# Kernel tuning notes

Hardware: AMD Instinct MI355X
Metric: run time of the kernel (lower is better)

Reference implementation:

```python
import jax, jax.numpy as jnp
import numpy as np

T, B, D, H = 4096, 4, 1024, 8
EPS = 1e-5


def _ln(z, g, b):
    m = jnp.mean(z, axis=-1, keepdims=True)
    v = jnp.mean((z - m) ** 2, axis=-1, keepdims=True)
    return (z - m) * jax.lax.rsqrt(v + EPS) * g + b


def setup_inputs() -> dict:
    key = jax.random.key(0)
    ks = jax.random.split(key, 8)
    s = 0.02
    return {
        "x": jax.random.normal(ks[0], (T, B, D), dtype=jnp.float32),
        "norm_w": jnp.ones((D,), jnp.float32),
        "norm_b": jnp.zeros((D,), jnp.float32),
        "tnorm_w": jnp.ones((D,), jnp.float32),
        "tnorm_b": jnp.zeros((D,), jnp.float32),
        "Wq": jax.random.normal(ks[1], (D, D), jnp.float32) * s,
        "bq": jnp.zeros((D,), jnp.float32),
        "Wk": jax.random.normal(ks[2], (D, D), jnp.float32) * s,
        "bk": jnp.zeros((D,), jnp.float32),
        "Wv": jax.random.normal(ks[3], (D, D), jnp.float32) * s,
        "bv": jnp.zeros((D,), jnp.float32),
    }


def reference(x, norm_w, norm_b, tnorm_w, tnorm_b, Wq, bq, Wk, bk, Wv, bv):
    # x: (T, B, D) -> (B, T, D), matching torch x.permute(1, 0, 2)
    xb = jnp.transpose(x, (1, 0, 2))
    b, t, d = xb.shape
    hd = d // H
    xn = _ln(xb, norm_w, norm_b)          # query branch norm
    xtn = _ln(xb, tnorm_w, tnorm_b)       # key/value branch norm (text_norm applied to x)
    q = (xn @ Wq.T + bq).reshape(b, t, H, hd)
    k = (xtn @ Wk.T + bk).reshape(b, t, H, hd)
    v = (xtn @ Wv.T + bv).reshape(b, t, H, hd)
    q = jax.nn.softmax(q, axis=-1)        # softmax over head-dim
    k = jax.nn.softmax(k, axis=1)         # softmax over time
    # kv state: (B, H, hd, hd)
    att = jnp.einsum('bthd,bthl->bhdl', k, v)
    y = jnp.einsum('bthd,bhdl->bthl', q, att).reshape(b, t, d)
    return y  # original forward returns y directly (proj_out/dropout unused)
```

## Files before the change

kernel.cpp:

```cpp
#include <hip/hip_runtime.h>
#include <cstdint>

#define T_LEN 4096
#define BATCH 4
#define DIM   1024
#define NH    8
#define HDIM  128
#define ROWS  16384

typedef __bf16 bf16x8 __attribute__((ext_vector_type(8)));
typedef float  f32x4  __attribute__((ext_vector_type(4)));

__device__ __forceinline__ unsigned short f2bf(float f) {
  union { float f; unsigned u; } a; a.f = f;
  unsigned u = a.u;
  u += 0x7fff + ((u >> 16) & 1);
  return (unsigned short)(u >> 16);
}
__device__ __forceinline__ float bf2f(unsigned short h) {
  union { unsigned u; float f; } a; a.u = ((unsigned)h) << 16;
  return a.f;
}

__device__ __forceinline__ void gld_lds16(const unsigned short* g, unsigned short* l) {
  __builtin_amdgcn_global_load_lds(
      (const __attribute__((address_space(1))) unsigned int*)g,
      (__attribute__((address_space(3))) unsigned int*)l, 16, 0, 0);
}

__global__ __launch_bounds__(256) void ln_kernel(
    const float* __restrict__ x, const float* __restrict__ nw, const float* __restrict__ nb,
    const float* __restrict__ tw, const float* __restrict__ tb,
    unsigned short* __restrict__ xn, unsigned short* __restrict__ xtn) {
  int row = blockIdx.x;
  int t = row >> 2, b = row & 3;
  int tid = threadIdx.x;
  const float4 v = ((const float4*)(x + (size_t)row * DIM))[tid];
  float s  = v.x + v.y + v.z + v.w;
  float s2 = v.x*v.x + v.y*v.y + v.z*v.z + v.w*v.w;
#pragma unroll
  for (int o = 32; o; o >>= 1) { s += __shfl_xor(s, o); s2 += __shfl_xor(s2, o); }
  __shared__ float red[8];
  int wv = tid >> 6;
  if ((tid & 63) == 0) { red[wv] = s; red[4 + wv] = s2; }
  __syncthreads();
  s  = red[0] + red[1] + red[2] + red[3];
  s2 = red[4] + red[5] + red[6] + red[7];
  float mean = s * (1.0f / DIM);
  float var  = s2 * (1.0f / DIM) - mean * mean;
  float rstd = rsqrtf(var + 1e-5f);
  size_t orow = ((size_t)b * T_LEN + t) * DIM;
  int c0 = tid * 4;
  float xv[4] = {v.x, v.y, v.z, v.w};
  union { unsigned short u[4]; uint2 d; } o1, o2;
#pragma unroll
  for (int j = 0; j < 4; ++j) {
    int c = c0 + j;
    float xh = (xv[j] - mean) * rstd;
    o1.u[j] = f2bf(xh * nw[c] + nb[c]);
    o2.u[j] = f2bf(xh * tw[c] + tb[c]);
  }
  *(uint2*)(xn  + orow + c0) = o1.d;
  *(uint2*)(xtn + orow + c0) = o2.d;
}

__global__ __launch_bounds__(256) void wconv(
    const float* __restrict__ Wq, const float* __restrict__ Wk, const float* __restrict__ Wv,
    unsigned short* __restrict__ out) {
  int i4 = blockIdx.x * 256 + threadIdx.x;
  int w = i4 >> 18;
  const float* src = (w == 0) ? Wq : (w == 1 ? Wk : Wv);
  float4 v = ((const float4*)src)[i4 & 262143];
  union { unsigned short u[4]; uint2 d; } o;
  o.u[0] = f2bf(v.x); o.u[1] = f2bf(v.y); o.u[2] = f2bf(v.z); o.u[3] = f2bf(v.w);
  ((uint2*)out)[i4] = o.d;
}

__global__ __launch_bounds__(256) void qkv_gemm(
    const unsigned short* __restrict__ xn, const unsigned short* __restrict__ xtn,
    const unsigned short* __restrict__ wbf,
    const float* __restrict__ bq, const float* __restrict__ bk, const float* __restrict__ bv,
    unsigned short* __restrict__ qo, unsigned short* __restrict__ ko, unsigned short* __restrict__ vo) {
  int z = blockIdx.z;
  const unsigned short* A = (z == 0) ? xn : xtn;
  const unsigned short* W = wbf + (size_t)z * DIM * DIM;
  const float* bias = (z == 0) ? bq : (z == 1 ? bk : bv);
  unsigned short* outp = (z == 0) ? qo : (z == 1 ? ko : vo);

  int m0t = blockIdx.x * 128;
  int n0 = blockIdx.y * 128;
  __shared__ __align__(16) unsigned short As[128 * 64];
  __shared__ __align__(16) unsigned short Bs[128 * 64];
  int tid = threadIdx.x;
  int wave = tid >> 6, lane = tid & 63;
  int wm = (wave >> 1) * 64, wn = (wave & 1) * 64;
  int l16 = lane & 15, kq = lane >> 4;
  int swz = l16 & 7;

  int srow = tid >> 3;
  int skk  = (((tid & 7) ^ ((tid >> 3) & 7)) * 8);
  const unsigned short* Ag = A + (size_t)(m0t + srow) * DIM + skk;
  const unsigned short* Wg = W + (size_t)(n0 + srow) * DIM + skk;
  unsigned short* Al = As + wave * 512;
  unsigned short* Bl = Bs + wave * 512;

  f32x4 acc[4][4] = {};

  for (int kt = 0; kt < DIM; kt += 64) {
#pragma unroll
    for (int p = 0; p < 4; ++p) {
      gld_lds16(Ag + (size_t)(p * 32) * DIM + kt, Al + p * 2048);
      gld_lds16(Wg + (size_t)(p * 32) * DIM + kt, Bl + p * 2048);
    }
    __syncthreads();
#pragma unroll
    for (int ks4 = 0; ks4 < 2; ++ks4) {
      int coff = (((kq + ks4 * 4) ^ swz) * 8);
      bf16x8 fa[4], fb[4];
#pragma unroll
      for (int i = 0; i < 4; ++i) {
        fa[i] = *(const bf16x8*)(As + (wm + i * 16 + l16) * 64 + coff);
        fb[i] = *(const bf16x8*)(Bs + (wn + i * 16 + l16) * 64 + coff);
      }
#pragma unroll
      for (int i = 0; i < 4; ++i)
#pragma unroll
        for (int j = 0; j < 4; ++j)
          acc[i][j] = __builtin_amdgcn_mfma_f32_16x16x32_bf16(fa[i], fb[j], acc[i][j], 0, 0, 0);
    }
    __syncthreads();
  }

  float bcol[4];
#pragma unroll
  for (int j = 0; j < 4; ++j) bcol[j] = bias[n0 + wn + j * 16 + l16];
#pragma unroll
  for (int i = 0; i < 4; ++i)
#pragma unroll
    for (int j = 0; j < 4; ++j)
#pragma unroll
      for (int r = 0; r < 4; ++r) acc[i][j][r] += bcol[j];

  if (z == 0) {
    float* redm = (float*)As;
    float* reds = redm + 256;
#pragma unroll
    for (int i = 0; i < 4; ++i) {
#pragma unroll
      for (int r = 0; r < 4; ++r) {
        float pm = acc[i][0][r];
#pragma unroll
        for (int j = 1; j < 4; ++j) pm = fmaxf(pm, acc[i][j][r]);
        pm = fmaxf(pm, __shfl_xor(pm, 1));
        pm = fmaxf(pm, __shfl_xor(pm, 2));
        pm = fmaxf(pm, __shfl_xor(pm, 4));
        pm = fmaxf(pm, __shfl_xor(pm, 8));
        float ps = 0.0f;
#pragma unroll
        for (int j = 0; j < 4; ++j) ps += __expf(acc[i][j][r] - pm);
        ps += __shfl_xor(ps, 1);
        ps += __shfl_xor(ps, 2);
        ps += __shfl_xor(ps, 4);
        ps += __shfl_xor(ps, 8);
        if (l16 == 0) {
          int lrow = wm + i * 16 + kq * 4 + r;
          redm[lrow * 2 + (wave & 1)] = pm;
          reds[lrow * 2 + (wave & 1)] = ps;
        }
      }
    }
    __syncthreads();
#pragma unroll
    for (int i = 0; i < 4; ++i) {
#pragma unroll
      for (int r = 0; r < 4; ++r) {
        int lrow = wm + i * 16 + kq * 4 + r;
        float ma = redm[lrow * 2], mb = redm[lrow * 2 + 1];
        float sa = reds[lrow * 2], sb = reds[lrow * 2 + 1];
        float M = fmaxf(ma, mb);
        float inv = 1.0f / (sa * __expf(ma - M) + sb * __expf(mb - M));
        size_t gr = (size_t)(m0t + lrow) * DIM;
#pragma unroll
        for (int j = 0; j < 4; ++j) {
          int col = n0 + wn + j * 16 + l16;
          outp[gr + col] = f2bf(__expf(acc[i][j][r] - M) * inv);
        }
      }
    }
  } else {
    int b = m0t >> 12;
    int tb = m0t & 4095;
    unsigned short* obase = outp + (size_t)b * DIM * T_LEN + tb;
    bool doExp = (z == 1);
#pragma unroll
    for (int j = 0; j < 4; ++j) {
      int col = n0 + wn + j * 16 + l16;
      unsigned short* cp = obase + (size_t)col * T_LEN;
#pragma unroll
      for (int i = 0; i < 4; ++i) {
        int t0 = wm + i * 16 + kq * 4;
#pragma unroll
        for (int r = 0; r < 4; ++r) {
          float val = acc[i][j][r];
          cp[t0 + r] = f2bf(doExp ? __expf(val) : val);
        }
      }
    }
  }
}

__global__ __launch_bounds__(256) void zsum(
    const unsigned short* __restrict__ ksmT, float* __restrict__ Zk) {
  int row = blockIdx.x;
  const unsigned short* p = ksmT + (size_t)row * T_LEN + threadIdx.x * 16;
  uint4 a = *(const uint4*)p;
  uint4 bq = *(const uint4*)(p + 8);
  const unsigned short* ua = (const unsigned short*)&a;
  const unsigned short* ub = (const unsigned short*)&bq;
  float s = 0.0f;
#pragma unroll
  for (int j = 0; j < 8; ++j) s += bf2f(ua[j]) + bf2f(ub[j]);
#pragma unroll
  for (int o = 32; o; o >>= 1) s += __shfl_xor(s, o);
  __shared__ float red[4];
  int wv = threadIdx.x >> 6;
  if ((threadIdx.x & 63) == 0) red[wv] = s;
  __syncthreads();
  if (threadIdx.x == 0) Zk[row] = red[0] + red[1] + red[2] + red[3];
}

__global__ __launch_bounds__(256) void att_gemm(
    const unsigned short* __restrict__ vT, const unsigned short* __restrict__ ksmT,
    float* __restrict__ attT) {
  int kc = blockIdx.x;
  int bh = blockIdx.y;
  const unsigned short* Arow = vT   + (size_t)bh * HDIM * T_LEN;
  const unsigned short* Brow = ksmT + (size_t)bh * HDIM * T_LEN;
  __shared__ __align__(16) unsigned short As[128 * 64];
  __shared__ __align__(16) unsigned short Bs[128 * 64];
  int tid = threadIdx.x;
  int wave = tid >> 6, lane = tid & 63;
  int wm = (wave >> 1) * 64, wn = (wave & 1) * 64;
  int l16 = lane & 15, kq = lane >> 4;
  int swz = l16 & 7;
  int srow = tid >> 3;
  int skk = (((tid & 7) ^ ((tid >> 3) & 7)) * 8);
  const unsigned short* Ag = Arow + (size_t)srow * T_LEN + skk;
  const unsigned short* Bg = Brow + (size_t)srow * T_LEN + skk;
  unsigned short* Al = As + wave * 512;
  unsigned short* Bl = Bs + wave * 512;
  f32x4 acc[4][4] = {};
  int kbeg = kc * 512;
  for (int kt = kbeg; kt < kbeg + 512; kt += 64) {
#pragma unroll
    for (int p = 0; p < 4; ++p) {
      gld_lds16(Ag + (size_t)(p * 32) * T_LEN + kt, Al + p * 2048);
      gld_lds16(Bg + (size_t)(p * 32) * T_LEN + kt, Bl + p * 2048);
    }
    __syncthreads();
#pragma unroll
    for (int ks4 = 0; ks4 < 2; ++ks4) {
      int coff = (((kq + ks4 * 4) ^ swz) * 8);
      bf16x8 fa[4], fb[4];
#pragma unroll
      for (int i = 0; i < 4; ++i) {
        fa[i] = *(const bf16x8*)(As + (wm + i * 16 + l16) * 64 + coff);
        fb[i] = *(const bf16x8*)(Bs + (wn + i * 16 + l16) * 64 + coff);
      }
#pragma unroll
      for (int i = 0; i < 4; ++i)
#pragma unroll
        for (int j = 0; j < 4; ++j)
          acc[i][j] = __builtin_amdgcn_mfma_f32_16x16x32_bf16(fa[i], fb[j], acc[i][j], 0, 0, 0);
    }
    __syncthreads();
  }
#pragma unroll
  for (int j = 0; j < 4; ++j) {
    int col = wn + j * 16 + l16;
#pragma unroll
    for (int i = 0; i < 4; ++i) {
      int rb = wm + i * 16 + kq * 4;
#pragma unroll
      for (int r = 0; r < 4; ++r)
        atomicAdd(attT + (size_t)bh * 16384 + (size_t)(rb + r) * 128 + col, acc[i][j][r]);
    }
  }
}

__global__ __launch_bounds__(256) void attcvt(
    const float* __restrict__ attT, const float* __restrict__ Zk,
    unsigned short* __restrict__ attbf) {
  int idx = blockIdx.x * 256 + threadIdx.x;
  int bh = idx >> 14;
  int b = bh >> 3, h = bh & 7;
  int d = idx & 127;
  float z = Zk[b * DIM + h * HDIM + d];
  attbf[idx] = f2bf(attT[idx] / z);
}

__global__ __launch_bounds__(256) void y_gemm(
    const unsigned short* __restrict__ qsm, const unsigned short* __restrict__ attbf,
    float* __restrict__ out) {
  int h = blockIdx.y;
  int m0t = blockIdx.x * 128;
  int b = m0t >> 12;
  int bh = b * 8 + h;
  const unsigned short* Brow = attbf + (size_t)bh * 16384;
  __shared__ __align__(16) unsigned short As[128 * 64];
  __shared__ __align__(16) unsigned short Bs[128 * 64];
  int tid = threadIdx.x;
  int wave = tid >> 6, lane = tid & 63;
  int wm = (wave >> 1) * 64, wn = (wave & 1) * 64;
  int l16 = lane & 15, kq = lane >> 4;
  int swz = l16 & 7;
  int srow = tid >> 3;
  int skk = (((tid & 7) ^ ((tid >> 3) & 7)) * 8);
  const unsigned short* Ag = qsm + (size_t)(m0t + srow) * DIM + h * HDIM + skk;
  const unsigned short* Bg = Brow + (size_t)srow * HDIM + skk;
  unsigned short* Al = As + wave * 512;
  unsigned short* Bl = Bs + wave * 512;
  f32x4 acc[4][4] = {};
  for (int kt = 0; kt < HDIM; kt += 64) {
#pragma unroll
    for (int p = 0; p < 4; ++p) {
      gld_lds16(Ag + (size_t)(p * 32) * DIM + kt, Al + p * 2048);
      gld_lds16(Bg + (size_t)(p * 32) * HDIM + kt, Bl + p * 2048);
    }
    __syncthreads();
#pragma unroll
    for (int ks4 = 0; ks4 < 2; ++ks4) {
      int coff = (((kq + ks4 * 4) ^ swz) * 8);
      bf16x8 fa[4], fb[4];
#pragma unroll
      for (int i = 0; i < 4; ++i) {
        fa[i] = *(const bf16x8*)(As + (wm + i * 16 + l16) * 64 + coff);
        fb[i] = *(const bf16x8*)(Bs + (wn + i * 16 + l16) * 64 + coff);
      }
#pragma unroll
      for (int i = 0; i < 4; ++i)
#pragma unroll
        for (int j = 0; j < 4; ++j)
          acc[i][j] = __builtin_amdgcn_mfma_f32_16x16x32_bf16(fa[i], fb[j], acc[i][j], 0, 0, 0);
    }
    __syncthreads();
  }
#pragma unroll
  for (int j = 0; j < 4; ++j) {
    int col = wn + j * 16 + l16;
#pragma unroll
    for (int i = 0; i < 4; ++i) {
      int rb = wm + i * 16 + kq * 4;
#pragma unroll
      for (int r = 0; r < 4; ++r)
        out[(size_t)(m0t + rb + r) * DIM + h * HDIM + col] = acc[i][j][r];
    }
  }
}

extern "C" void kernel_launch(void* const* d_in, const int* in_sizes, int n_in,
                              void* d_out, int out_size, void* d_ws, size_t ws_size,
                              hipStream_t stream) {
  const float* x  = (const float*)d_in[0];
  const float* nw = (const float*)d_in[1];
  const float* nb = (const float*)d_in[2];
  const float* tw = (const float*)d_in[3];
  const float* tb = (const float*)d_in[4];
  const float* Wq = (const float*)d_in[5];
  const float* bq = (const float*)d_in[6];
  const float* Wk = (const float*)d_in[7];
  const float* bk = (const float*)d_in[8];
  const float* Wv = (const float*)d_in[9];
  const float* bv = (const float*)d_in[10];
  float* out = (float*)d_out;

  char* ws = (char*)d_ws;
  unsigned short* xn   = (unsigned short*)(ws);
  unsigned short* xtn  = (unsigned short*)(ws + 33554432);
  unsigned short* q    = (unsigned short*)(ws + 67108864);
  unsigned short* ksmT = (unsigned short*)(ws + 100663296);
  unsigned short* vT   = (unsigned short*)(ws + 134217728);
  unsigned short* wbf  = (unsigned short*)(ws + 167772160);
  float* attT          = (float*)(ws + 174063616);
  unsigned short* attbf= (unsigned short*)(ws + 176160768);
  float* Zk            = (float*)(ws + 177209344);

  ln_kernel<<<ROWS, 256, 0, stream>>>(x, nw, nb, tw, tb, xn, xtn);
  wconv<<<3072, 256, 0, stream>>>(Wq, Wk, Wv, wbf);
  qkv_gemm<<<dim3(128, 8, 3), 256, 0, stream>>>(xn, xtn, wbf, bq, bk, bv, q, ksmT, vT);
  zsum<<<4096, 256, 0, stream>>>(ksmT, Zk);
  (void)hipMemsetAsync(attT, 0, 32 * 128 * 128 * 4, stream);
  att_gemm<<<dim3(8, 32), 256, 0, stream>>>(vT, ksmT, attT);
  attcvt<<<2048, 256, 0, stream>>>(attT, Zk, attbf);
  y_gemm<<<dim3(128, 8), 256, 0, stream>>>(q, attbf, out);
}
```

Measured before the change: 339.5 us.

## Enlarge QKV GEMM tile to 256x256 with double-buffered LDS pipeline

Reworks the QKV projection GEMM to use 512-thread blocks computing 256x256 output tiles. Global-to-LDS loads go through a two-stage double buffer with explicit vmcnt waits, and s_setprio is set around the MFMA bursts. The goal is to overlap memory loads with MFMA work and to raise data reuse per byte loaded. The V/K transposed output stores are packed into 8-byte vector writes. The change uses 128KB of LDS and 128 accumulator registers per lane, which limits occupancy to one block per CU and spreads the head-dim softmax reduction across wave pairs.

```diff
diff --git a/kernel.cpp b/kernel.cpp
--- a/kernel.cpp
+++ b/kernel.cpp
@@ -76,7 +76,7 @@
   ((uint2*)out)[i4] = o.d;
 }
 
-__global__ __launch_bounds__(256) void qkv_gemm(
+__global__ __launch_bounds__(512, 2) void qkv_gemm(
     const unsigned short* __restrict__ xn, const unsigned short* __restrict__ xtn,
     const unsigned short* __restrict__ wbf,
     const float* __restrict__ bq, const float* __restrict__ bk, const float* __restrict__ bv,
@@ -87,109 +87,135 @@
   const float* bias = (z == 0) ? bq : (z == 1 ? bk : bv);
   unsigned short* outp = (z == 0) ? qo : (z == 1 ? ko : vo);
 
-  int m0t = blockIdx.x * 128;
-  int n0 = blockIdx.y * 128;
-  __shared__ __align__(16) unsigned short As[128 * 64];
-  __shared__ __align__(16) unsigned short Bs[128 * 64];
+  int m0 = blockIdx.x * 256;
+  int n0 = blockIdx.y * 256;
+
+  __shared__ __align__(16) unsigned short lds[65536];
+
   int tid = threadIdx.x;
   int wave = tid >> 6, lane = tid & 63;
-  int wm = (wave >> 1) * 64, wn = (wave & 1) * 64;
+  int wr = wave >> 2, wc = wave & 3;
+  int wm = wr * 128, wn = wc * 64;
   int l16 = lane & 15, kq = lane >> 4;
   int swz = l16 & 7;
 
   int srow = tid >> 3;
   int skk  = (((tid & 7) ^ ((tid >> 3) & 7)) * 8);
-  const unsigned short* Ag = A + (size_t)(m0t + srow) * DIM + skk;
+  const unsigned short* Ag = A + (size_t)(m0 + srow) * DIM + skk;
   const unsigned short* Wg = W + (size_t)(n0 + srow) * DIM + skk;
-  unsigned short* Al = As + wave * 512;
-  unsigned short* Bl = Bs + wave * 512;
-
-  f32x4 acc[4][4] = {};
-
-  for (int kt = 0; kt < DIM; kt += 64) {
+
+  f32x4 acc[8][4] = {};
+
+  auto stage = [&](int tt, int sb) {
+    int kt = tt * 64;
 #pragma unroll
     for (int p = 0; p < 4; ++p) {
-      gld_lds16(Ag + (size_t)(p * 32) * DIM + kt, Al + p * 2048);
-      gld_lds16(Wg + (size_t)(p * 32) * DIM + kt, Bl + p * 2048);
-    }
-    __syncthreads();
-#pragma unroll
-    for (int ks4 = 0; ks4 < 2; ++ks4) {
+      gld_lds16(Ag + (size_t)(p * 64) * DIM + kt, lds + sb + p * 4096 + wave * 512);
+      gld_lds16(Wg + (size_t)(p * 64) * DIM + kt, lds + 32768 + sb + p * 4096 + wave * 512);
+    }
+  };
+
+  stage(0, 0);
+  stage(1, 16384);
+
+  for (int t = 0; t < 16; ++t) {
+    int sb = (t & 1) ? 16384 : 0;
+    const unsigned short* As = lds + sb;
+    const unsigned short* Bs = lds + 32768 + sb;
+
+    if (t < 15) asm volatile("s_waitcnt vmcnt(8)" ::: "memory");
+    else        asm volatile("s_waitcnt vmcnt(0)" ::: "memory");
+    __builtin_amdgcn_sched_barrier(0);
+    __builtin_amdgcn_s_barrier();
+    __builtin_amdgcn_sched_barrier(0);
+
+#pragma unroll
+    for (int ph = 0; ph < 4; ++ph) {
+      int mh = ph & 1, ks4 = ph >> 1;
       int coff = (((kq + ks4 * 4) ^ swz) * 8);
       bf16x8 fa[4], fb[4];
 #pragma unroll
       for (int i = 0; i < 4; ++i) {
-        fa[i] = *(const bf16x8*)(As + (wm + i * 16 + l16) * 64 + coff);
+        fa[i] = *(const bf16x8*)(As + (wm + (mh * 4 + i) * 16 + l16) * 64 + coff);
         fb[i] = *(const bf16x8*)(Bs + (wn + i * 16 + l16) * 64 + coff);
       }
+      __builtin_amdgcn_s_barrier();
+      __builtin_amdgcn_s_setprio(1);
 #pragma unroll
       for (int i = 0; i < 4; ++i)
 #pragma unroll
         for (int j = 0; j < 4; ++j)
-          acc[i][j] = __builtin_amdgcn_mfma_f32_16x16x32_bf16(fa[i], fb[j], acc[i][j], 0, 0, 0);
-    }
-    __syncthreads();
-  }
-
-  float bcol[4];
-#pragma unroll
-  for (int j = 0; j < 4; ++j) bcol[j] = bias[n0 + wn + j * 16 + l16];
-#pragma unroll
-  for (int i = 0; i < 4; ++i)
-#pragma unroll
-    for (int j = 0; j < 4; ++j)
-#pragma unroll
-      for (int r = 0; r < 4; ++r) acc[i][j][r] += bcol[j];
+          acc[mh * 4 + i][j] =
+              __builtin_amdgcn_mfma_f32_16x16x32_bf16(fa[i], fb[j], acc[mh * 4 + i][j], 0, 0, 0);
+      __builtin_amdgcn_s_setprio(0);
+      __builtin_amdgcn_s_barrier();
+    }
+
+    asm volatile("" ::: "memory");
+    __builtin_amdgcn_sched_barrier(0);
+    if (t < 14) stage(t + 2, sb);
+    __builtin_amdgcn_sched_barrier(0);
+  }
+
+#pragma unroll
+  for (int j = 0; j < 4; ++j) {
+    float bc = bias[n0 + wn + j * 16 + l16];
+#pragma unroll
+    for (int ii = 0; ii < 8; ++ii)
+#pragma unroll
+      for (int r = 0; r < 4; ++r) acc[ii][j][r] += bc;
+  }
 
   if (z == 0) {
-    float* redm = (float*)As;
-    float* reds = redm + 256;
-#pragma unroll
-    for (int i = 0; i < 4; ++i) {
+    float* redm = (float*)lds;
+    float* reds = redm + 1024;
+#pragma unroll
+    for (int ii = 0; ii < 8; ++ii) {
 #pragma unroll
       for (int r = 0; r < 4; ++r) {
-        float pm = acc[i][0][r];
-#pragma unroll
-        for (int j = 1; j < 4; ++j) pm = fmaxf(pm, acc[i][j][r]);
+        float pm = acc[ii][0][r];
+#pragma unroll
+        for (int j = 1; j < 4; ++j) pm = fmaxf(pm, acc[ii][j][r]);
         pm = fmaxf(pm, __shfl_xor(pm, 1));
         pm = fmaxf(pm, __shfl_xor(pm, 2));
         pm = fmaxf(pm, __shfl_xor(pm, 4));
         pm = fmaxf(pm, __shfl_xor(pm, 8));
         float ps = 0.0f;
 #pragma unroll
-        for (int j = 0; j < 4; ++j) ps += __expf(acc[i][j][r] - pm);
+        for (int j = 0; j < 4; ++j) ps += __expf(acc[ii][j][r] - pm);
         ps += __shfl_xor(ps, 1);
         ps += __shfl_xor(ps, 2);
         ps += __shfl_xor(ps, 4);
         ps += __shfl_xor(ps, 8);
         if (l16 == 0) {
-          int lrow = wm + i * 16 + kq * 4 + r;
-          redm[lrow * 2 + (wave & 1)] = pm;
-          reds[lrow * 2 + (wave & 1)] = ps;
+          int row = wm + ii * 16 + kq * 4 + r;
+          redm[row * 4 + wc] = pm;
+          reds[row * 4 + wc] = ps;
         }
       }
     }
     __syncthreads();
 #pragma unroll
-    for (int i = 0; i < 4; ++i) {
+    for (int ii = 0; ii < 8; ++ii) {
 #pragma unroll
       for (int r = 0; r < 4; ++r) {
-        int lrow = wm + i * 16 + kq * 4 + r;
-        float ma = redm[lrow * 2], mb = redm[lrow * 2 + 1];
-        float sa = reds[lrow * 2], sb = reds[lrow * 2 + 1];
+        int row = wm + ii * 16 + kq * 4 + r;
+        int pb = wc & 2;
+        float ma = redm[row * 4 + pb], mb = redm[row * 4 + pb + 1];
+        float sa = reds[row * 4 + pb], sb2 = reds[row * 4 + pb + 1];
         float M = fmaxf(ma, mb);
-        float inv = 1.0f / (sa * __expf(ma - M) + sb * __expf(mb - M));
-        size_t gr = (size_t)(m0t + lrow) * DIM;
+        float inv = 1.0f / (sa * __expf(ma - M) + sb2 * __expf(mb - M));
+        size_t gr = (size_t)(m0 + row) * DIM;
 #pragma unroll
         for (int j = 0; j < 4; ++j) {
           int col = n0 + wn + j * 16 + l16;
-          outp[gr + col] = f2bf(__expf(acc[i][j][r] - M) * inv);
+          outp[gr + col] = f2bf(__expf(acc[ii][j][r] - M) * inv);
         }
       }
     }
   } else {
-    int b = m0t >> 12;
-    int tb = m0t & 4095;
+    int b = m0 >> 12;
+    int tb = m0 & 4095;
     unsigned short* obase = outp + (size_t)b * DIM * T_LEN + tb;
     bool doExp = (z == 1);
 #pragma unroll
@@ -197,13 +223,15 @@
       int col = n0 + wn + j * 16 + l16;
       unsigned short* cp = obase + (size_t)col * T_LEN;
 #pragma unroll
-      for (int i = 0; i < 4; ++i) {
-        int t0 = wm + i * 16 + kq * 4;
+      for (int ii = 0; ii < 8; ++ii) {
+        int t0 = wm + ii * 16 + kq * 4;
+        union { unsigned short u[4]; uint2 d; } o;
 #pragma unroll
         for (int r = 0; r < 4; ++r) {
-          float val = acc[i][j][r];
-          cp[t0 + r] = f2bf(doExp ? __expf(val) : val);
+          float val = acc[ii][j][r];
+          o.u[r] = f2bf(doExp ? __expf(val) : val);
         }
+        *(uint2*)(cp + t0) = o.d;
       }
     }
   }
@@ -387,7 +415,7 @@
 
   ln_kernel<<<ROWS, 256, 0, stream>>>(x, nw, nb, tw, tb, xn, xtn);
   wconv<<<3072, 256, 0, stream>>>(Wq, Wk, Wv, wbf);
-  qkv_gemm<<<dim3(128, 8, 3), 256, 0, stream>>>(xn, xtn, wbf, bq, bk, bv, q, ksmT, vT);
+  qkv_gemm<<<dim3(64, 4, 3), 512, 0, stream>>>(xn, xtn, wbf, bq, bk, bv, q, ksmT, vT);
   zsum<<<4096, 256, 0, stream>>>(ksmT, Zk);
   (void)hipMemsetAsync(attT, 0, 32 * 128 * 128 * 4, stream);
   att_gemm<<<dim3(8, 32), 256, 0, stream>>>(vT, ksmT, attT);
```

After: 333.9 us. About the same (-1.7%).

## Double-buffer QKV GEMM, fuse weight conversion into LN, fold Z sums into epilogue

Applied to the files above, without the earlier changes.

The QKV GEMM now runs 512-thread blocks over 256-row tiles with a K-step of 32. Two LDS buffers are filled asynchronously and explicit vmcnt waits plus barriers overlap loads with MFMA. The weight bf16 conversion becomes extra blocks of the LayerNorm kernel, and the separate zsum pass is replaced by per-column exp sums reduced with shuffles and atomically added into Zk in the GEMM epilogue. The K/V stores are also vectorised into 8-byte writes. This removes two launches and a full reread of the key tensor, at the cost of atomics and the risk that the hand-tuned waitcnt pipeline is fragile.

```diff
diff --git a/kernel.cpp b/kernel.cpp
--- a/kernel.cpp
+++ b/kernel.cpp
@@ -28,13 +28,25 @@
       (__attribute__((address_space(3))) unsigned int*)l, 16, 0, 0);
 }
 
-__global__ __launch_bounds__(256) void ln_kernel(
+__global__ __launch_bounds__(256) void lnw_kernel(
     const float* __restrict__ x, const float* __restrict__ nw, const float* __restrict__ nb,
     const float* __restrict__ tw, const float* __restrict__ tb,
-    unsigned short* __restrict__ xn, unsigned short* __restrict__ xtn) {
+    unsigned short* __restrict__ xn, unsigned short* __restrict__ xtn,
+    const float* __restrict__ Wq, const float* __restrict__ Wk, const float* __restrict__ Wv,
+    unsigned short* __restrict__ wbf) {
+  int tid = threadIdx.x;
+  if (blockIdx.x >= ROWS) {
+    int i4 = (blockIdx.x - ROWS) * 256 + tid;
+    int w = i4 >> 18;
+    const float* src = (w == 0) ? Wq : (w == 1 ? Wk : Wv);
+    float4 v = ((const float4*)src)[i4 & 262143];
+    union { unsigned short u[4]; uint2 d; } o;
+    o.u[0] = f2bf(v.x); o.u[1] = f2bf(v.y); o.u[2] = f2bf(v.z); o.u[3] = f2bf(v.w);
+    ((uint2*)wbf)[i4] = o.d;
+    return;
+  }
   int row = blockIdx.x;
   int t = row >> 2, b = row & 3;
-  int tid = threadIdx.x;
   const float4 v = ((const float4*)(x + (size_t)row * DIM))[tid];
   float s  = v.x + v.y + v.z + v.w;
   float s2 = v.x*v.x + v.y*v.y + v.z*v.z + v.w*v.w;
@@ -64,86 +76,89 @@
   *(uint2*)(xtn + orow + c0) = o2.d;
 }
 
-__global__ __launch_bounds__(256) void wconv(
-    const float* __restrict__ Wq, const float* __restrict__ Wk, const float* __restrict__ Wv,
-    unsigned short* __restrict__ out) {
-  int i4 = blockIdx.x * 256 + threadIdx.x;
-  int w = i4 >> 18;
-  const float* src = (w == 0) ? Wq : (w == 1 ? Wk : Wv);
-  float4 v = ((const float4*)src)[i4 & 262143];
-  union { unsigned short u[4]; uint2 d; } o;
-  o.u[0] = f2bf(v.x); o.u[1] = f2bf(v.y); o.u[2] = f2bf(v.z); o.u[3] = f2bf(v.w);
-  ((uint2*)out)[i4] = o.d;
-}
-
-__global__ __launch_bounds__(256) void qkv_gemm(
+__global__ __launch_bounds__(512, 4) void qkv_gemm(
     const unsigned short* __restrict__ xn, const unsigned short* __restrict__ xtn,
     const unsigned short* __restrict__ wbf,
     const float* __restrict__ bq, const float* __restrict__ bk, const float* __restrict__ bv,
-    unsigned short* __restrict__ qo, unsigned short* __restrict__ ko, unsigned short* __restrict__ vo) {
+    unsigned short* __restrict__ qo, unsigned short* __restrict__ ko, unsigned short* __restrict__ vo,
+    float* __restrict__ Zk) {
   int z = blockIdx.z;
   const unsigned short* A = (z == 0) ? xn : xtn;
   const unsigned short* W = wbf + (size_t)z * DIM * DIM;
   const float* bias = (z == 0) ? bq : (z == 1 ? bk : bv);
   unsigned short* outp = (z == 0) ? qo : (z == 1 ? ko : vo);
 
-  int m0t = blockIdx.x * 128;
+  int m0 = blockIdx.x * 256;
   int n0 = blockIdx.y * 128;
-  __shared__ __align__(16) unsigned short As[128 * 64];
-  __shared__ __align__(16) unsigned short Bs[128 * 64];
+
+  __shared__ __align__(16) unsigned short lds[24576];
+
   int tid = threadIdx.x;
   int wave = tid >> 6, lane = tid & 63;
-  int wm = (wave >> 1) * 64, wn = (wave & 1) * 64;
+  int wr = wave >> 1, wc = wave & 1;
+  int wm = wr * 64, wn = wc * 64;
   int l16 = lane & 15, kq = lane >> 4;
-  int swz = l16 & 7;
-
-  int srow = tid >> 3;
-  int skk  = (((tid & 7) ^ ((tid >> 3) & 7)) * 8);
-  const unsigned short* Ag = A + (size_t)(m0t + srow) * DIM + skk;
-  const unsigned short* Wg = W + (size_t)(n0 + srow) * DIM + skk;
-  unsigned short* Al = As + wave * 512;
-  unsigned short* Bl = Bs + wave * 512;
+  int rs = (kq ^ (l16 & 3)) * 8;
+
+  int arow = tid >> 2;
+  int achk = (tid & 3) ^ (arow & 3);
+  const unsigned short* Ag = A + (size_t)(m0 + arow) * DIM + achk * 8;
+  const unsigned short* Wg = W + (size_t)(n0 + arow) * DIM + achk * 8;
 
   f32x4 acc[4][4] = {};
 
-  for (int kt = 0; kt < DIM; kt += 64) {
-#pragma unroll
-    for (int p = 0; p < 4; ++p) {
-      gld_lds16(Ag + (size_t)(p * 32) * DIM + kt, Al + p * 2048);
-      gld_lds16(Wg + (size_t)(p * 32) * DIM + kt, Bl + p * 2048);
-    }
-    __syncthreads();
-#pragma unroll
-    for (int ks4 = 0; ks4 < 2; ++ks4) {
-      int coff = (((kq + ks4 * 4) ^ swz) * 8);
-      bf16x8 fa[4], fb[4];
-#pragma unroll
-      for (int i = 0; i < 4; ++i) {
-        fa[i] = *(const bf16x8*)(As + (wm + i * 16 + l16) * 64 + coff);
-        fb[i] = *(const bf16x8*)(Bs + (wn + i * 16 + l16) * 64 + coff);
-      }
-#pragma unroll
-      for (int i = 0; i < 4; ++i)
-#pragma unroll
-        for (int j = 0; j < 4; ++j)
-          acc[i][j] = __builtin_amdgcn_mfma_f32_16x16x32_bf16(fa[i], fb[j], acc[i][j], 0, 0, 0);
-    }
-    __syncthreads();
-  }
-
-  float bcol[4];
-#pragma unroll
-  for (int j = 0; j < 4; ++j) bcol[j] = bias[n0 + wn + j * 16 + l16];
-#pragma unroll
-  for (int i = 0; i < 4; ++i)
-#pragma unroll
-    for (int j = 0; j < 4; ++j)
-#pragma unroll
-      for (int r = 0; r < 4; ++r) acc[i][j][r] += bcol[j];
+  auto stage = [&](int tt, int sb) {
+    int kt = tt * 32;
+    gld_lds16(Ag + kt,                  lds + sb + wave * 512);
+    gld_lds16(Ag + (size_t)128 * DIM + kt, lds + sb + 4096 + wave * 512);
+    gld_lds16(Wg + kt,                  lds + sb + 8192 + wave * 512);
+  };
+
+  stage(0, 0);
+  stage(1, 12288);
+
+  for (int t = 0; t < 32; ++t) {
+    int sb = (t & 1) ? 12288 : 0;
+    const unsigned short* As = lds + sb;
+    const unsigned short* Bs = lds + sb + 8192;
+
+    if (t < 31) asm volatile("s_waitcnt vmcnt(3)" ::: "memory");
+    else        asm volatile("s_waitcnt vmcnt(0)" ::: "memory");
+    __builtin_amdgcn_sched_barrier(0);
+    __builtin_amdgcn_s_barrier();
+    __builtin_amdgcn_sched_barrier(0);
+
+    bf16x8 fa[4], fb[4];
+#pragma unroll
+    for (int i = 0; i < 4; ++i) {
+      fa[i] = *(const bf16x8*)(As + (wm + i * 16 + l16) * 32 + rs);
+      fb[i] = *(const bf16x8*)(Bs + (wn + i * 16 + l16) * 32 + rs);
+    }
+#pragma unroll
+    for (int i = 0; i < 4; ++i)
+#pragma unroll
+      for (int j = 0; j < 4; ++j)
+        acc[i][j] = __builtin_amdgcn_mfma_f32_16x16x32_bf16(fa[i], fb[j], acc[i][j], 0, 0, 0);
+
+    __builtin_amdgcn_sched_barrier(0);
+    __builtin_amdgcn_s_barrier();
+    __builtin_amdgcn_sched_barrier(0);
+    if (t < 30) stage(t + 2, sb);
+    __builtin_amdgcn_sched_barrier(0);
+  }
+
+#pragma unroll
+  for (int j = 0; j < 4; ++j) {
+    float bc = bias[n0 + wn + j * 16 + l16];
+#pragma unroll
+    for (int i = 0; i < 4; ++i)
+#pragma unroll
+      for (int r = 0; r < 4; ++r) acc[i][j][r] += bc;
+  }
 
   if (z == 0) {
-    float* redm = (float*)As;
-    float* reds = redm + 256;
+    float* redm = (float*)lds;
+    float* reds = redm + 512;
 #pragma unroll
     for (int i = 0; i < 4; ++i) {
 #pragma unroll
@@ -163,9 +178,9 @@
         ps += __shfl_xor(ps, 4);
         ps += __shfl_xor(ps, 8);
         if (l16 == 0) {
-          int lrow = wm + i * 16 + kq * 4 + r;
-          redm[lrow * 2 + (wave & 1)] = pm;
-          reds[lrow * 2 + (wave & 1)] = ps;
+          int row = wm + i * 16 + kq * 4 + r;
+          redm[row * 2 + wc] = pm;
+          reds[row * 2 + wc] = ps;
         }
       }
     }
@@ -174,12 +189,12 @@
     for (int i = 0; i < 4; ++i) {
 #pragma unroll
       for (int r = 0; r < 4; ++r) {
-        int lrow = wm + i * 16 + kq * 4 + r;
-        float ma = redm[lrow * 2], mb = redm[lrow * 2 + 1];
-        float sa = reds[lrow * 2], sb = reds[lrow * 2 + 1];
+        int row = wm + i * 16 + kq * 4 + r;
+        float ma = redm[row * 2], mb = redm[row * 2 + 1];
+        float sa = reds[row * 2], sb2 = reds[row * 2 + 1];
         float M = fmaxf(ma, mb);
-        float inv = 1.0f / (sa * __expf(ma - M) + sb * __expf(mb - M));
-        size_t gr = (size_t)(m0t + lrow) * DIM;
+        float inv = 1.0f / (sa * __expf(ma - M) + sb2 * __expf(mb - M));
+        size_t gr = (size_t)(m0 + row) * DIM;
 #pragma unroll
         for (int j = 0; j < 4; ++j) {
           int col = n0 + wn + j * 16 + l16;
@@ -188,10 +203,11 @@
       }
     }
   } else {
-    int b = m0t >> 12;
-    int tb = m0t & 4095;
+    int b = m0 >> 12;
+    int tb = m0 & 4095;
     unsigned short* obase = outp + (size_t)b * DIM * T_LEN + tb;
     bool doExp = (z == 1);
+    float zs[4] = {0.0f, 0.0f, 0.0f, 0.0f};
 #pragma unroll
     for (int j = 0; j < 4; ++j) {
       int col = n0 + wn + j * 16 + l16;
@@ -199,34 +215,28 @@
 #pragma unroll
       for (int i = 0; i < 4; ++i) {
         int t0 = wm + i * 16 + kq * 4;
+        union { unsigned short u[4]; uint2 d; } o;
 #pragma unroll
         for (int r = 0; r < 4; ++r) {
           float val = acc[i][j][r];
-          cp[t0 + r] = f2bf(doExp ? __expf(val) : val);
+          if (doExp) { val = __expf(val); zs[j] += val; }
+          o.u[r] = f2bf(val);
         }
-      }
-    }
-  }
-}
-
-__global__ __launch_bounds__(256) void zsum(
-    const unsigned short* __restrict__ ksmT, float* __restrict__ Zk) {
-  int row = blockIdx.x;
-  const unsigned short* p = ksmT + (size_t)row * T_LEN + threadIdx.x * 16;
-  uint4 a = *(const uint4*)p;
-  uint4 bq = *(const uint4*)(p + 8);
-  const unsigned short* ua = (const unsigned short*)&a;
-  const unsigned short* ub = (const unsigned short*)&bq;
-  float s = 0.0f;
-#pragma unroll
-  for (int j = 0; j < 8; ++j) s += bf2f(ua[j]) + bf2f(ub[j]);
-#pragma unroll
-  for (int o = 32; o; o >>= 1) s += __shfl_xor(s, o);
-  __shared__ float red[4];
-  int wv = threadIdx.x >> 6;
-  if ((threadIdx.x & 63) == 0) red[wv] = s;
-  __syncthreads();
-  if (threadIdx.x == 0) Zk[row] = red[0] + red[1] + red[2] + red[3];
+        *(uint2*)(cp + t0) = o.d;
+      }
+    }
+    if (doExp) {
+#pragma unroll
+      for (int j = 0; j < 4; ++j) {
+        zs[j] += __shfl_xor(zs[j], 16);
+        zs[j] += __shfl_xor(zs[j], 32);
+        if (kq == 0) {
+          int col = n0 + wn + j * 16 + l16;
+          atomicAdd(Zk + b * DIM + col, zs[j]);
+        }
+      }
+    }
+  }
 }
 
 __global__ __launch_bounds__(256) void att_gemm(
@@ -385,11 +395,10 @@
   unsigned short* attbf= (unsigned short*)(ws + 176160768);
   float* Zk            = (float*)(ws + 177209344);
 
-  ln_kernel<<<ROWS, 256, 0, stream>>>(x, nw, nb, tw, tb, xn, xtn);
-  wconv<<<3072, 256, 0, stream>>>(Wq, Wk, Wv, wbf);
-  qkv_gemm<<<dim3(128, 8, 3), 256, 0, stream>>>(xn, xtn, wbf, bq, bk, bv, q, ksmT, vT);
-  zsum<<<4096, 256, 0, stream>>>(ksmT, Zk);
   (void)hipMemsetAsync(attT, 0, 32 * 128 * 128 * 4, stream);
+  (void)hipMemsetAsync(Zk, 0, BATCH * DIM * 4, stream);
+  lnw_kernel<<<ROWS + 3072, 256, 0, stream>>>(x, nw, nb, tw, tb, xn, xtn, Wq, Wk, Wv, wbf);
+  qkv_gemm<<<dim3(64, 8, 3), 512, 0, stream>>>(xn, xtn, wbf, bq, bk, bv, q, ksmT, vT, Zk);
   att_gemm<<<dim3(8, 32), 256, 0, stream>>>(vT, ksmT, attT);
   attcvt<<<2048, 256, 0, stream>>>(attT, Zk, attbf);
   y_gemm<<<dim3(128, 8), 256, 0, stream>>>(q, attbf, out);
```

New measurement: 322.7 us. -5.0%, faster.
